# Kernel tuning notes

Hardware: AMD Instinct MI355X
Metric: run time of the kernel (lower is better)

Reference implementation:

```python
import jax, jax.numpy as jnp
import numpy as np

B, N, FIN, FOUT = 32, 1024, 128, 128
NEG_SLOPE = 0.01  # torch nn.LeakyReLU default


def setup_inputs() -> dict:
    key = jax.random.key(0)
    k1, k2, k3, k4 = jax.random.split(key, 4)
    node_mat = jax.random.normal(k1, (B, N, FIN), dtype=jnp.float32)
    adj_mat = jax.random.uniform(k2, (B, N, N), dtype=jnp.float32)
    # nn.Linear(FIN, FOUT): weight [FOUT, FIN], bias [FOUT]
    bound = 1.0 / np.sqrt(FIN)
    W = jax.random.uniform(k3, (FOUT, FIN), minval=-bound, maxval=bound, dtype=jnp.float32)
    b = jax.random.uniform(k4, (FOUT,), minval=-bound, maxval=bound, dtype=jnp.float32)
    return {"node_mat": node_mat, "adj_mat": adj_mat, "W": W, "b": b}


def reference(node_mat, adj_mat, W, b):
    # degree per node: row-sum of adjacency [B, N, 1]
    n_neighbors = adj_mat.sum(axis=-1, keepdims=True)
    # D^-1 A : the original builds eye*(1/deg) then bmm; algebraically a row scaling
    norm_adj = adj_mat / n_neighbors                      # [B, N, N]
    agg = jnp.einsum('bnm,bmf->bnf', norm_adj, node_mat)  # [B, N, FIN]
    out = jnp.einsum('bnf,of->bno', agg, W) + b           # [B, N, FOUT]
    return jnp.where(out >= 0, out, NEG_SLOPE * out)      # LeakyReLU
```

## Files before the change

### kernel.cpp

```cpp
#include <hip/hip_runtime.h>
#include <cstdint>
#include <cstddef>

#define BB   32
#define NN   1024
#define FIN  128
#define FOUT 128

typedef __attribute__((ext_vector_type(8))) short bf16x8;
typedef __attribute__((ext_vector_type(4))) float f32x4;

__device__ __forceinline__ unsigned int f2bf(float f) {
    union { float f; unsigned int u; } v; v.f = f;
    unsigned int u = v.u;
    return (u + 0x7FFFu + ((u >> 16) & 1u)) >> 16;
}
__device__ __forceinline__ unsigned int pack2(float a, float b) {
    return f2bf(a) | (f2bf(b) << 16);
}

__device__ __forceinline__ void load_lds16(const void* g, void* l) {
    __builtin_amdgcn_global_load_lds(
        (const __attribute__((address_space(1))) unsigned int*)g,
        (__attribute__((address_space(3))) unsigned int*)l, 16, 0, 0);
}

__global__ __launch_bounds__(256) void y_kernel(const float* __restrict__ node,
                                                const float* __restrict__ W,
                                                unsigned short* __restrict__ Yt) {
    __shared__ unsigned short Wlds[128 * 136];
    __shared__ unsigned short Nlds[64 * 136];

    const int tid = threadIdx.x;
    const int bid = blockIdx.x;
    const int b   = bid >> 4;
    const int m0  = (bid & 15) * 64;

    #pragma unroll
    for (int i = 0; i < 16; ++i) {
        const int idx = i * 256 + tid;
        const int row = idx >> 5;
        const int c   = (idx & 31) * 4;
        float4 v = ((const float4*)W)[idx];
        uint2 p; p.x = pack2(v.x, v.y); p.y = pack2(v.z, v.w);
        *(uint2*)&Wlds[row * 136 + c] = p;
    }
    {
        const float* base = node + ((size_t)b * NN + m0) * FIN;
        #pragma unroll
        for (int i = 0; i < 8; ++i) {
            const int idx = i * 256 + tid;
            const int row = idx >> 5;
            const int c   = (idx & 31) * 4;
            float4 v = *(const float4*)(base + row * FIN + c);
            uint2 p; p.x = pack2(v.x, v.y); p.y = pack2(v.z, v.w);
            *(uint2*)&Nlds[row * 136 + c] = p;
        }
    }
    __syncthreads();

    const int w = tid >> 6, lane = tid & 63;
    const int wo = w * 32;
    const int lcol = lane & 15, lk = (lane >> 4) * 8;

    f32x4 acc[2][4] = {};
    #pragma unroll
    for (int kc = 0; kc < 4; ++kc) {
        const int kof = kc * 32 + lk;
        bf16x8 a[2], bb[4];
        #pragma unroll
        for (int mi = 0; mi < 2; ++mi)
            a[mi] = *(const bf16x8*)&Wlds[(wo + mi*16 + lcol) * 136 + kof];
        #pragma unroll
        for (int ni = 0; ni < 4; ++ni)
            bb[ni] = *(const bf16x8*)&Nlds[(ni*16 + lcol) * 136 + kof];
        #pragma unroll
        for (int mi = 0; mi < 2; ++mi)
            #pragma unroll
            for (int ni = 0; ni < 4; ++ni)
                acc[mi][ni] = __builtin_amdgcn_mfma_f32_16x16x32_bf16(
                    a[mi], bb[ni], acc[mi][ni], 0, 0, 0);
    }
    __syncthreads();

    unsigned short* Ylds = Wlds;
    const int rq = (lane >> 4) * 4;
    #pragma unroll
    for (int mi = 0; mi < 2; ++mi)
        #pragma unroll
        for (int ni = 0; ni < 4; ++ni)
            #pragma unroll
            for (int r = 0; r < 4; ++r) {
                const int o = wo + mi * 16 + rq + r;
                const int m = ni * 16 + lcol;
                Ylds[o * 72 + m] = (unsigned short)f2bf(acc[mi][ni][r]);
            }
    __syncthreads();

    {
        const int oq = tid >> 3, c = (tid & 7) * 8;
        #pragma unroll
        for (int j = 0; j < 4; ++j) {
            const int o = oq + 32 * j;
            uint4 v = *(const uint4*)&Ylds[o * 72 + c];
            *(uint4*)(Yt + ((size_t)b * FOUT + o) * NN + m0 + c) = v;
        }
    }
}

#define BUFB 12288

__global__ __launch_bounds__(256, 4) void gcn_kernel(const float* __restrict__ adj,
                                                     const unsigned short* __restrict__ Yt,
                                                     const float* __restrict__ bias,
                                                     float* __restrict__ out) {
    __shared__ char smem[2 * BUFB];

    const int tid  = threadIdx.x;
    const int lane = tid & 63;
    const int w    = tid >> 6;

    const int raw = blockIdx.x;
    const int bid = (raw & 7) * 128 + (raw >> 3);
    const int b   = bid >> 5;
    const int n0  = (bid & 31) * 32;

    const int lcol = lane & 15, q = lane >> 4;
    const int wm = (w & 1) * 16;
    const int wn = (w >> 1) * 64;

    const int rA = w * 8 + (lane >> 3);
    const int gA = (lane & 7) ^ (lane >> 3);
    const float* aSrc = adj + ((size_t)(b * NN + n0 + rA)) * NN + gA * 4;
    char* aDst = smem + w * 1024;

    const unsigned short* bSrc[2];
    char* bDst[2];
    #pragma unroll
    for (int j = 0; j < 2; ++j) {
        const int s = (w * 2 + j) * 64 + lane;
        const int o = s >> 2, c = s & 3;
        const int g = c ^ (o & 3);
        bSrc[j] = Yt + ((size_t)(b * FOUT + o)) * NN + g * 8;
        bDst[j] = smem + 4096 + (w * 2 + j) * 1024;
    }

    const int R = wm + lcol, keyA = R & 7;
    const int offA0 = (R * 8 + ((2 * q)     ^ keyA)) * 16;
    const int offA1 = (R * 8 + ((2 * q + 1) ^ keyA)) * 16;
    int offB[4];
    #pragma unroll
    for (int ni = 0; ni < 4; ++ni) {
        const int o = wn + ni * 16 + lcol;
        offB[ni] = 4096 + (o * 4 + (q ^ (o & 3))) * 16;
    }

    f32x4 acc[4] = {};
    float rsum = 0.f;

    #define STAGE(buf, s)                                                  \
        do {                                                               \
            load_lds16(aSrc    + (s) * 32, aDst    + (buf) * BUFB);        \
            load_lds16(bSrc[0] + (s) * 32, bDst[0] + (buf) * BUFB);        \
            load_lds16(bSrc[1] + (s) * 32, bDst[1] + (buf) * BUFB);        \
        } while (0)

    #define COMPUTE(buf)                                                   \
        do {                                                               \
            const char* base = smem + (buf) * BUFB;                        \
            const float4 f0 = *(const float4*)(base + offA0);              \
            const float4 f1 = *(const float4*)(base + offA1);              \
            rsum += ((f0.x + f0.y) + (f0.z + f0.w))                        \
                  + ((f1.x + f1.y) + (f1.z + f1.w));                       \
            uint4 pk;                                                      \
            pk.x = pack2(f0.x, f0.y); pk.y = pack2(f0.z, f0.w);            \
            pk.z = pack2(f1.x, f1.y); pk.w = pack2(f1.z, f1.w);            \
            const bf16x8 a = *(const bf16x8*)&pk;                          \
            _Pragma("unroll")                                              \
            for (int ni = 0; ni < 4; ++ni) {                               \
                const bf16x8 bbf = *(const bf16x8*)(base + offB[ni]);      \
                acc[ni] = __builtin_amdgcn_mfma_f32_16x16x32_bf16(         \
                    a, bbf, acc[ni], 0, 0, 0);                             \
            }                                                              \
        } while (0)

    STAGE(0, 0);
    asm volatile("s_waitcnt vmcnt(0)" ::: "memory");
    __builtin_amdgcn_s_barrier();

    for (int t = 0; t < 16; ++t) {
        STAGE(1, 2 * t + 1);
        COMPUTE(0);
        asm volatile("s_waitcnt vmcnt(0)" ::: "memory");
        __builtin_amdgcn_s_barrier();

        if (t < 15) STAGE(0, 2 * t + 2);
        COMPUTE(1);
        asm volatile("s_waitcnt vmcnt(0)" ::: "memory");
        __builtin_amdgcn_s_barrier();
    }
    #undef STAGE
    #undef COMPUTE

    rsum += __shfl_xor(rsum, 16);
    rsum += __shfl_xor(rsum, 32);

    const int rq = q * 4;
    float sc[4];
    #pragma unroll
    for (int r = 0; r < 4; ++r) sc[r] = 1.0f / __shfl(rsum, rq + r);

    float* outB = out + ((size_t)(b * NN + n0 + wm)) * FOUT;
    #pragma unroll
    for (int ni = 0; ni < 4; ++ni) {
        const float bc = bias[wn + ni * 16 + lcol];
        #pragma unroll
        for (int r = 0; r < 4; ++r) {
            float v = acc[ni][r] * sc[r] + bc;
            v = (v >= 0.f) ? v : 0.01f * v;
            outB[(size_t)(rq + r) * FOUT + wn + ni * 16 + lcol] = v;
        }
    }
}

extern "C" void kernel_launch(void* const* d_in, const int* in_sizes, int n_in,
                              void* d_out, int out_size, void* d_ws, size_t ws_size,
                              hipStream_t stream) {
    const float* node = (const float*)d_in[0];
    const float* adj  = (const float*)d_in[1];
    const float* W    = (const float*)d_in[2];
    const float* bias = (const float*)d_in[3];
    float* out = (float*)d_out;
    unsigned short* Yt = (unsigned short*)d_ws;

    hipLaunchKernelGGL(y_kernel,   dim3(512),  dim3(256), 0, stream, node, W, Yt);
    hipLaunchKernelGGL(gcn_kernel, dim3(1024), dim3(256), 0, stream, adj, Yt, bias, out);
}
```

Measured before the change: 234.9 us.

## Replace direct global-to-LDS loads with register-staged prefetch two stages ahead

Replaces the global_load_lds async copies with ordinary global loads into registers, then ds_write into a padded (non-swizzled) LDS layout. The loop now prefetches tile t+2 into registers while tile t is computed and t+1 is written to LDS, so the barrier waits only on LDS traffic and not on outstanding global loads. The cost is extra VGPRs and explicit LDS writes, plus a padded layout that replaces the XOR swizzle. There is also a hazard: the barrier before each DSWRITE only waits on lgkmcnt, which may not correctly order the write against the previous compute's reads of the same buffer.

```diff
diff --git a/kernel.cpp b/kernel.cpp
--- a/kernel.cpp
+++ b/kernel.cpp
@@ -17,12 +17,6 @@
 }
 __device__ __forceinline__ unsigned int pack2(float a, float b) {
     return f2bf(a) | (f2bf(b) << 16);
-}
-
-__device__ __forceinline__ void load_lds16(const void* g, void* l) {
-    __builtin_amdgcn_global_load_lds(
-        (const __attribute__((address_space(1))) unsigned int*)g,
-        (__attribute__((address_space(3))) unsigned int*)l, 16, 0, 0);
 }
 
 __global__ __launch_bounds__(256) void y_kernel(const float* __restrict__ node,
@@ -108,13 +102,15 @@
     }
 }
 
-#define BUFB 12288
+#define ABYTES 4608
+#define BBYTES 10240
+#define BUFB   (ABYTES + BBYTES)
 
 __global__ __launch_bounds__(256, 4) void gcn_kernel(const float* __restrict__ adj,
                                                      const unsigned short* __restrict__ Yt,
                                                      const float* __restrict__ bias,
                                                      float* __restrict__ out) {
-    __shared__ char smem[2 * BUFB];
+    __shared__ __align__(16) char smem[2 * BUFB];
 
     const int tid  = threadIdx.x;
     const int lane = tid & 63;
@@ -129,47 +125,55 @@
     const int wm = (w & 1) * 16;
     const int wn = (w >> 1) * 64;
 
-    const int rA = w * 8 + (lane >> 3);
-    const int gA = (lane & 7) ^ (lane >> 3);
-    const float* aSrc = adj + ((size_t)(b * NN + n0 + rA)) * NN + gA * 4;
-    char* aDst = smem + w * 1024;
+    const int grA = w * 8 + (lane >> 3);
+    const int gcA = lane & 7;
+    const float* aSrc = adj + ((size_t)(b * NN + n0 + grA)) * NN + gcA * 4;
+    const int aWoff = (grA * 36 + gcA * 4) * 4;
 
     const unsigned short* bSrc[2];
-    char* bDst[2];
+    int bWoff[2];
     #pragma unroll
     for (int j = 0; j < 2; ++j) {
-        const int s = (w * 2 + j) * 64 + lane;
-        const int o = s >> 2, c = s & 3;
-        const int g = c ^ (o & 3);
-        bSrc[j] = Yt + ((size_t)(b * FOUT + o)) * NN + g * 8;
-        bDst[j] = smem + 4096 + (w * 2 + j) * 1024;
-    }
-
-    const int R = wm + lcol, keyA = R & 7;
-    const int offA0 = (R * 8 + ((2 * q)     ^ keyA)) * 16;
-    const int offA1 = (R * 8 + ((2 * q + 1) ^ keyA)) * 16;
+        const int o  = (w * 2 + j) * 16 + (lane >> 2);
+        const int kc = lane & 3;
+        bSrc[j]  = Yt + ((size_t)(b * FOUT + o)) * NN + kc * 8;
+        bWoff[j] = ABYTES + o * 80 + kc * 16;
+    }
+
+    const int R = wm + lcol;
+    const int offA0 = (R * 36 + q * 8) * 4;
     int offB[4];
     #pragma unroll
     for (int ni = 0; ni < 4; ++ni) {
         const int o = wn + ni * 16 + lcol;
-        offB[ni] = 4096 + (o * 4 + (q ^ (o & 3))) * 16;
+        offB[ni] = ABYTES + o * 80 + q * 16;
     }
 
     f32x4 acc[4] = {};
     float rsum = 0.f;
 
-    #define STAGE(buf, s)                                                  \
+    float4 ra; uint4 rb0, rb1;
+
+    #define GLOAD(s)                                                       \
         do {                                                               \
-            load_lds16(aSrc    + (s) * 32, aDst    + (buf) * BUFB);        \
-            load_lds16(bSrc[0] + (s) * 32, bDst[0] + (buf) * BUFB);        \
-            load_lds16(bSrc[1] + (s) * 32, bDst[1] + (buf) * BUFB);        \
+            ra  = *(const float4*)(aSrc    + (s) * 32);                    \
+            rb0 = *(const uint4*)(bSrc[0] + (s) * 32);                     \
+            rb1 = *(const uint4*)(bSrc[1] + (s) * 32);                     \
+        } while (0)
+
+    #define DSWRITE(buf)                                                   \
+        do {                                                               \
+            char* base = smem + (buf) * BUFB;                              \
+            *(float4*)(base + aWoff)    = ra;                              \
+            *(uint4*)(base + bWoff[0]) = rb0;                              \
+            *(uint4*)(base + bWoff[1]) = rb1;                              \
         } while (0)
 
     #define COMPUTE(buf)                                                   \
         do {                                                               \
             const char* base = smem + (buf) * BUFB;                        \
             const float4 f0 = *(const float4*)(base + offA0);              \
-            const float4 f1 = *(const float4*)(base + offA1);              \
+            const float4 f1 = *(const float4*)(base + offA0 + 16);         \
             rsum += ((f0.x + f0.y) + (f0.z + f0.w))                        \
                   + ((f1.x + f1.y) + (f1.z + f1.w));                       \
             uint4 pk;                                                      \
@@ -184,22 +188,25 @@
             }                                                              \
         } while (0)
 
-    STAGE(0, 0);
-    asm volatile("s_waitcnt vmcnt(0)" ::: "memory");
+    GLOAD(0);
+    DSWRITE(0);
+    GLOAD(1);
+    asm volatile("s_waitcnt lgkmcnt(0)" ::: "memory");
     __builtin_amdgcn_s_barrier();
 
-    for (int t = 0; t < 16; ++t) {
-        STAGE(1, 2 * t + 1);
-        COMPUTE(0);
-        asm volatile("s_waitcnt vmcnt(0)" ::: "memory");
-        __builtin_amdgcn_s_barrier();
-
-        if (t < 15) STAGE(0, 2 * t + 2);
-        COMPUTE(1);
-        asm volatile("s_waitcnt vmcnt(0)" ::: "memory");
-        __builtin_amdgcn_s_barrier();
-    }
-    #undef STAGE
+    #pragma unroll 2
+    for (int t = 0; t < 32; ++t) {
+        const int cur = t & 1, nxt = cur ^ 1;
+        if (t < 31) DSWRITE(nxt);
+        if (t < 30) GLOAD(t + 2);
+        COMPUTE(cur);
+        if (t < 31) {
+            asm volatile("s_waitcnt lgkmcnt(0)" ::: "memory");
+            __builtin_amdgcn_s_barrier();
+        }
+    }
+    #undef GLOAD
+    #undef DSWRITE
     #undef COMPUTE
 
     rsum += __shfl_xor(rsum, 16);
```

After: 239.7 us. 1.02x slower.

## Enlarge GCN block tile to 128 rows with 1024 threads and deeper K step

Applied to the files above, without the earlier changes.

The aggregation kernel now processes 128 adjacency rows per block with 16 waves, instead of 32 rows with 4 waves, and stages 64 K-columns per pipeline step. This cuts the number of times each batch's transposed Y matrix is re-read from global memory by four, and halves the number of loop iterations and barriers. The double-buffered pipeline is restructured to wait on only the older stage's loads. The cost is a much larger LDS footprint (96KB) and one block per CU, which reduces latency hiding from running multiple blocks per CU.

```diff
diff --git a/kernel.cpp b/kernel.cpp
--- a/kernel.cpp
+++ b/kernel.cpp
@@ -108,51 +108,61 @@
     }
 }
 
-#define BUFB 12288
-
-__global__ __launch_bounds__(256, 4) void gcn_kernel(const float* __restrict__ adj,
-                                                     const unsigned short* __restrict__ Yt,
-                                                     const float* __restrict__ bias,
-                                                     float* __restrict__ out) {
-    __shared__ char smem[2 * BUFB];
+#define ABYTES 32768
+#define BBYTES 16384
+#define BUFB   (ABYTES + BBYTES)
+
+__global__ __launch_bounds__(1024, 4) void gcn_kernel(const float* __restrict__ adj,
+                                                      const unsigned short* __restrict__ Yt,
+                                                      const float* __restrict__ bias,
+                                                      float* __restrict__ out) {
+    __shared__ __align__(16) char smem[2 * BUFB];
 
     const int tid  = threadIdx.x;
     const int lane = tid & 63;
     const int w    = tid >> 6;
 
     const int raw = blockIdx.x;
-    const int bid = (raw & 7) * 128 + (raw >> 3);
-    const int b   = bid >> 5;
-    const int n0  = (bid & 31) * 32;
+    const int bid = (raw & 7) * 32 + (raw >> 3);
+    const int b   = bid >> 3;
+    const int n0  = (bid & 7) * 128;
 
     const int lcol = lane & 15, q = lane >> 4;
-    const int wm = (w & 1) * 16;
-    const int wn = (w >> 1) * 64;
-
-    const int rA = w * 8 + (lane >> 3);
-    const int gA = (lane & 7) ^ (lane >> 3);
-    const float* aSrc = adj + ((size_t)(b * NN + n0 + rA)) * NN + gA * 4;
-    char* aDst = smem + w * 1024;
-
-    const unsigned short* bSrc[2];
-    char* bDst[2];
+    const int wm = (w & 7) * 16;
+    const int wn = (w >> 3) * 64;
+
+    const float* aSrc[2];
+    char*        aDst[2];
     #pragma unroll
     for (int j = 0; j < 2; ++j) {
-        const int s = (w * 2 + j) * 64 + lane;
-        const int o = s >> 2, c = s & 3;
-        const int g = c ^ (o & 3);
-        bSrc[j] = Yt + ((size_t)(b * FOUT + o)) * NN + g * 8;
-        bDst[j] = smem + 4096 + (w * 2 + j) * 1024;
-    }
-
-    const int R = wm + lcol, keyA = R & 7;
-    const int offA0 = (R * 8 + ((2 * q)     ^ keyA)) * 16;
-    const int offA1 = (R * 8 + ((2 * q + 1) ^ keyA)) * 16;
-    int offB[4];
-    #pragma unroll
-    for (int ni = 0; ni < 4; ++ni) {
-        const int o = wn + ni * 16 + lcol;
-        offB[ni] = 4096 + (o * 4 + (q ^ (o & 3))) * 16;
+        const int i  = w * 2 + j;
+        const int rA = i * 4 + (lane >> 4);
+        const int c  = lane & 15;
+        const int g  = (c & 8) | ((c & 7) ^ (rA & 7));
+        aSrc[j] = adj + ((size_t)(b * NN + n0 + rA)) * NN + g * 4;
+        aDst[j] = smem + i * 1024;
+    }
+    const unsigned short* bSrc;
+    char* bDst;
+    {
+        const int o = w * 8 + (lane >> 3);
+        const int c = lane & 7;
+        const int g = c ^ (o & 7);
+        bSrc = Yt + ((size_t)(b * FOUT + o)) * NN + g * 8;
+        bDst = smem + ABYTES + w * 1024;
+    }
+
+    const int R = wm + lcol, keyR = R & 7;
+    int offA[2][2], offB[2][4];
+    #pragma unroll
+    for (int kcl = 0; kcl < 2; ++kcl) {
+        offA[kcl][0] = (R * 16 + kcl * 8 + ((2 * q)     ^ keyR)) * 16;
+        offA[kcl][1] = (R * 16 + kcl * 8 + ((2 * q + 1) ^ keyR)) * 16;
+        #pragma unroll
+        for (int ni = 0; ni < 4; ++ni) {
+            const int o = wn + ni * 16 + lcol;
+            offB[kcl][ni] = ABYTES + (o * 8 + ((kcl * 4 + q) ^ (o & 7))) * 16;
+        }
     }
 
     f32x4 acc[4] = {};
@@ -160,27 +170,30 @@
 
     #define STAGE(buf, s)                                                  \
         do {                                                               \
-            load_lds16(aSrc    + (s) * 32, aDst    + (buf) * BUFB);        \
-            load_lds16(bSrc[0] + (s) * 32, bDst[0] + (buf) * BUFB);        \
-            load_lds16(bSrc[1] + (s) * 32, bDst[1] + (buf) * BUFB);        \
+            load_lds16(aSrc[0] + (s) * 64, aDst[0] + (buf) * BUFB);        \
+            load_lds16(aSrc[1] + (s) * 64, aDst[1] + (buf) * BUFB);        \
+            load_lds16(bSrc    + (s) * 64, bDst    + (buf) * BUFB);        \
         } while (0)
 
     #define COMPUTE(buf)                                                   \
         do {                                                               \
             const char* base = smem + (buf) * BUFB;                        \
-            const float4 f0 = *(const float4*)(base + offA0);              \
-            const float4 f1 = *(const float4*)(base + offA1);              \
-            rsum += ((f0.x + f0.y) + (f0.z + f0.w))                        \
-                  + ((f1.x + f1.y) + (f1.z + f1.w));                       \
-            uint4 pk;                                                      \
-            pk.x = pack2(f0.x, f0.y); pk.y = pack2(f0.z, f0.w);            \
-            pk.z = pack2(f1.x, f1.y); pk.w = pack2(f1.z, f1.w);            \
-            const bf16x8 a = *(const bf16x8*)&pk;                          \
             _Pragma("unroll")                                              \
-            for (int ni = 0; ni < 4; ++ni) {                               \
-                const bf16x8 bbf = *(const bf16x8*)(base + offB[ni]);      \
-                acc[ni] = __builtin_amdgcn_mfma_f32_16x16x32_bf16(         \
-                    a, bbf, acc[ni], 0, 0, 0);                             \
+            for (int kcl = 0; kcl < 2; ++kcl) {                            \
+                const float4 f0 = *(const float4*)(base + offA[kcl][0]);   \
+                const float4 f1 = *(const float4*)(base + offA[kcl][1]);   \
+                rsum += ((f0.x + f0.y) + (f0.z + f0.w))                    \
+                      + ((f1.x + f1.y) + (f1.z + f1.w));                   \
+                uint4 pk;                                                  \
+                pk.x = pack2(f0.x, f0.y); pk.y = pack2(f0.z, f0.w);        \
+                pk.z = pack2(f1.x, f1.y); pk.w = pack2(f1.z, f1.w);        \
+                const bf16x8 a = *(const bf16x8*)&pk;                      \
+                _Pragma("unroll")                                          \
+                for (int ni = 0; ni < 4; ++ni) {                           \
+                    const bf16x8 bbf = *(const bf16x8*)(base + offB[kcl][ni]); \
+                    acc[ni] = __builtin_amdgcn_mfma_f32_16x16x32_bf16(     \
+                        a, bbf, acc[ni], 0, 0, 0);                         \
+                }                                                          \
             }                                                              \
         } while (0)
 
@@ -188,16 +201,18 @@
     asm volatile("s_waitcnt vmcnt(0)" ::: "memory");
     __builtin_amdgcn_s_barrier();
 
+    #pragma unroll 2
     for (int t = 0; t < 16; ++t) {
-        STAGE(1, 2 * t + 1);
-        COMPUTE(0);
-        asm volatile("s_waitcnt vmcnt(0)" ::: "memory");
+        const int cur = t & 1, nxt = cur ^ 1;
+        if (t < 15) {
+            STAGE(nxt, t + 1);
+            asm volatile("s_waitcnt vmcnt(3)" ::: "memory");
+        } else {
+            asm volatile("s_waitcnt vmcnt(0)" ::: "memory");
+        }
         __builtin_amdgcn_s_barrier();
-
-        if (t < 15) STAGE(0, 2 * t + 2);
-        COMPUTE(1);
-        asm volatile("s_waitcnt vmcnt(0)" ::: "memory");
-        __builtin_amdgcn_s_barrier();
+        COMPUTE(cur);
+        if (t < 15) __builtin_amdgcn_s_barrier();
     }
     #undef STAGE
     #undef COMPUTE
@@ -233,6 +248,6 @@
     float* out = (float*)d_out;
     unsigned short* Yt = (unsigned short*)d_ws;
 
-    hipLaunchKernelGGL(y_kernel,   dim3(512),  dim3(256), 0, stream, node, W, Yt);
-    hipLaunchKernelGGL(gcn_kernel, dim3(1024), dim3(256), 0, stream, adj, Yt, bias, out);
-}
+    hipLaunchKernelGGL(y_kernel,   dim3(512), dim3(256),  0, stream, node, W, Yt);
+    hipLaunchKernelGGL(gcn_kernel, dim3(256), dim3(1024), 0, stream, adj, Yt, bias, out);
+}
```

Result: faster. 225.9 us (-3.9%).
